# Performance work log

Measured on AMD Instinct MI355X. Metric: run time of the kernel, lower is better.

The kernel has to match this reference:

```python
import jax, jax.numpy as jnp
import numpy as np

BIG = 1000000.0
EPS = 1e-06
COST_CLASS, COST_BBOX, COST_GIOU = 1.0, 5.0, 2.0


def sanitize_boxes(boxes):
    # boxes: [..., 4] cxcywh
    boxes = jnp.nan_to_num(boxes, nan=0.0, posinf=1.0, neginf=0.0)
    cx, cy, w, h = jnp.moveaxis(boxes, -1, 0)
    cx = jnp.clip(cx, 0.0, 1.0)
    cy = jnp.clip(cy, 0.0, 1.0)
    w = jnp.clip(w, EPS, 1.0)
    h = jnp.clip(h, EPS, 1.0)
    return jnp.stack([cx, cy, w, h], axis=-1)


def box_cxcywh_to_xyxy(x):
    cx, cy, w, h = jnp.moveaxis(x, -1, 0)
    return jnp.stack([cx - 0.5 * w, cy - 0.5 * h, cx + 0.5 * w, cy + 0.5 * h], axis=-1)


def pairwise_giou(b1, b2):
    # b1: [B, Q, 4] xyxy, b2: [B, T, 4] xyxy -> [B, Q, T]
    area1 = (b1[..., 2] - b1[..., 0]) * (b1[..., 3] - b1[..., 1])  # [B,Q]
    area2 = (b2[..., 2] - b2[..., 0]) * (b2[..., 3] - b2[..., 1])  # [B,T]
    lt = jnp.maximum(b1[:, :, None, :2], b2[:, None, :, :2])  # [B,Q,T,2]
    rb = jnp.minimum(b1[:, :, None, 2:], b2[:, None, :, 2:])
    wh = jnp.clip(rb - lt, 0.0)
    inter = wh[..., 0] * wh[..., 1]  # [B,Q,T]
    union = area1[:, :, None] + area2[:, None, :] - inter
    iou = inter / union
    # enclosing box
    lt_c = jnp.minimum(b1[:, :, None, :2], b2[:, None, :, :2])
    rb_c = jnp.maximum(b1[:, :, None, 2:], b2[:, None, :, 2:])
    wh_c = jnp.clip(rb_c - lt_c, 0.0)
    area_c = wh_c[..., 0] * wh_c[..., 1]
    return iou - (area_c - union) / area_c


def reference(pred_logits, pred_boxes, tgt_labels, tgt_boxes):
    # Batched cost-matrix construction of HungarianMatcher.forward.
    out_logits = jnp.nan_to_num(pred_logits, nan=0.0, posinf=0.0, neginf=0.0)
    out_prob = jax.nn.softmax(out_logits, axis=-1)  # [B,Q,C]
    out_bbox = sanitize_boxes(pred_boxes)           # [B,Q,4]
    t_bbox = sanitize_boxes(tgt_boxes)              # [B,T,4]

    # cost_class[b,q,t] = -out_prob[b,q,tgt_labels[b,t]]
    B, Q, C = out_prob.shape
    T = tgt_labels.shape[1]
    gather_idx = jnp.broadcast_to(tgt_labels[:, None, :], (B, Q, T))
    cost_class = -jnp.take_along_axis(out_prob, gather_idx, axis=2)  # [B,Q,T]

    # L1 cdist in cxcywh space
    cost_bbox = jnp.sum(jnp.abs(out_bbox[:, :, None, :] - t_bbox[:, None, :, :]), axis=-1)

    cost_giou = -pairwise_giou(box_cxcywh_to_xyxy(out_bbox), box_cxcywh_to_xyxy(t_bbox))

    Cmat = COST_CLASS * cost_class + COST_BBOX * cost_bbox + COST_GIOU * cost_giou
    return jnp.nan_to_num(Cmat, nan=BIG, posinf=BIG, neginf=BIG)


def setup_inputs() -> dict:
    key = jax.random.key(0)
    k1, k2, k3, k4 = jax.random.split(key, 4)
    B, Q, C, T = 64, 900, 256, 200
    return {
        "pred_logits": jax.random.normal(k1, (B, Q, C), dtype=jnp.float32),
        "pred_boxes": jax.random.uniform(k2, (B, Q, 4), dtype=jnp.float32),
        "tgt_labels": jax.random.randint(k3, (B, T), 0, C),
        "tgt_boxes": jax.random.uniform(k4, (B, T, 4), dtype=jnp.float32),
    }
```

## Files before the change

### kernel.cpp

```cpp
#include <hip/hip_runtime.h>
#include <math.h>

constexpr int B = 64, Q = 900, C = 256, T = 200;
constexpr float BIG = 1000000.0f;
constexpr float EPSV = 1e-6f;
constexpr int WAVES_PER_BLOCK = 4;
constexpr int QPB = WAVES_PER_BLOCK;

__device__ __forceinline__ float fix_logit(float x) {
    unsigned u = __float_as_uint(x);
    return ((u & 0x7f800000u) == 0x7f800000u) ? 0.0f : x;
}

__device__ __forceinline__ float fix_box(float x) {
    unsigned u = __float_as_uint(x);
    if ((u & 0x7f800000u) == 0x7f800000u) {
        if (u & 0x007fffffu) return 0.0f;
        return (u & 0x80000000u) ? 0.0f : 1.0f;
    }
    return x;
}

__device__ __forceinline__ float clampf(float x, float lo, float hi) {
    return fminf(fmaxf(x, lo), hi);
}

__global__ __launch_bounds__(256, 2)
void matcher_kernel(const float* __restrict__ logits,
                    const float* __restrict__ pboxes,
                    const int*   __restrict__ tlabels,
                    const float* __restrict__ tboxes,
                    float* __restrict__ out)
{
    __shared__ float s_tx0[T], s_ty0[T], s_tx1[T], s_ty1[T], s_tarea[T];
    __shared__ float s_tcx[T], s_tcy[T], s_tw[T], s_th[T];
    __shared__ int   s_tlab[T];
    __shared__ float s_exp[WAVES_PER_BLOCK][C];

    const int blocks_per_b = Q / QPB;
    const int b    = blockIdx.x / blocks_per_b;
    const int qblk = blockIdx.x % blocks_per_b;
    const int tid  = threadIdx.x;
    const int wave = tid >> 6;
    const int lane = tid & 63;
    const int q    = qblk * QPB + wave;

    for (int t = tid; t < T; t += blockDim.x) {
        float4 tb = ((const float4*)(tboxes + (size_t)b * T * 4))[t];
        float cx = clampf(fix_box(tb.x), 0.0f, 1.0f);
        float cy = clampf(fix_box(tb.y), 0.0f, 1.0f);
        float w  = clampf(fix_box(tb.z), EPSV, 1.0f);
        float h  = clampf(fix_box(tb.w), EPSV, 1.0f);
        s_tcx[t] = cx; s_tcy[t] = cy; s_tw[t] = w; s_th[t] = h;
        float x0 = cx - 0.5f * w, y0 = cy - 0.5f * h;
        float x1 = cx + 0.5f * w, y1 = cy + 0.5f * h;
        s_tx0[t] = x0; s_ty0[t] = y0; s_tx1[t] = x1; s_ty1[t] = y1;
        s_tarea[t] = (x1 - x0) * (y1 - y0);
        int lab = tlabels[(size_t)b * T + t];
        s_tlab[t] = min(max(lab, 0), C - 1);
    }

    const size_t row = (size_t)b * Q + q;
    const float4 lg4 = ((const float4*)(logits + row * C))[lane];
    float l0 = fix_logit(lg4.x), l1 = fix_logit(lg4.y);
    float l2 = fix_logit(lg4.z), l3 = fix_logit(lg4.w);

    float m = fmaxf(fmaxf(l0, l1), fmaxf(l2, l3));
    #pragma unroll
    for (int off = 32; off > 0; off >>= 1)
        m = fmaxf(m, __shfl_xor(m, off));

    float e0 = __expf(l0 - m), e1 = __expf(l1 - m);
    float e2 = __expf(l2 - m), e3 = __expf(l3 - m);
    float s = (e0 + e1) + (e2 + e3);
    #pragma unroll
    for (int off = 32; off > 0; off >>= 1)
        s += __shfl_xor(s, off);
    const float inv_sum = 1.0f / s;

    ((float4*)&s_exp[wave][0])[lane] = make_float4(e0, e1, e2, e3);

    const float4 pb = *(const float4*)(pboxes + row * 4);
    float pcx = clampf(fix_box(pb.x), 0.0f, 1.0f);
    float pcy = clampf(fix_box(pb.y), 0.0f, 1.0f);
    float pw  = clampf(fix_box(pb.z), EPSV, 1.0f);
    float ph  = clampf(fix_box(pb.w), EPSV, 1.0f);
    float px0 = pcx - 0.5f * pw, py0 = pcy - 0.5f * ph;
    float px1 = pcx + 0.5f * pw, py1 = pcy + 0.5f * ph;
    float parea = (px1 - px0) * (py1 - py0);

    __syncthreads();

    float* orow = out + row * T;
    for (int t = lane; t < T; t += 64) {
        float prob = s_exp[wave][s_tlab[t]] * inv_sum;

        float l1c = fabsf(pcx - s_tcx[t]) + fabsf(pcy - s_tcy[t])
                  + fabsf(pw  - s_tw[t])  + fabsf(ph  - s_th[t]);

        float ltx = fmaxf(px0, s_tx0[t]), lty = fmaxf(py0, s_ty0[t]);
        float rbx = fminf(px1, s_tx1[t]), rby = fminf(py1, s_ty1[t]);
        float iw = fmaxf(rbx - ltx, 0.0f), ih = fmaxf(rby - lty, 0.0f);
        float inter = iw * ih;
        float uni = parea + s_tarea[t] - inter;
        float iou = inter / uni;

        float cx0 = fminf(px0, s_tx0[t]), cy0 = fminf(py0, s_ty0[t]);
        float cx1 = fmaxf(px1, s_tx1[t]), cy1 = fmaxf(py1, s_ty1[t]);
        float cw = fmaxf(cx1 - cx0, 0.0f), ch = fmaxf(cy1 - cy0, 0.0f);
        float ca = cw * ch;
        float giou = iou - (ca - uni) / ca;

        float cost = -prob + 5.0f * l1c - 2.0f * giou;
        unsigned cu = __float_as_uint(cost);
        if ((cu & 0x7f800000u) == 0x7f800000u) cost = BIG;
        orow[t] = cost;
    }
}

extern "C" void kernel_launch(void* const* d_in, const int* in_sizes, int n_in,
                              void* d_out, int out_size, void* d_ws, size_t ws_size,
                              hipStream_t stream) {
    const float* logits  = (const float*)d_in[0];
    const float* pboxes  = (const float*)d_in[1];
    const int*   tlabels = (const int*)d_in[2];
    const float* tboxes  = (const float*)d_in[3];
    float* out = (float*)d_out;

    dim3 grid(B * (Q / QPB));
    dim3 block(64 * WAVES_PER_BLOCK);
    matcher_kernel<<<grid, block, 0, stream>>>(logits, pboxes, tlabels, tboxes, out);
}
```

Baseline: 123.4 us.

## Process eight queries per wave with target boxes held in registers

Each wave now handles eight query rows instead of one. Target boxes and label offsets are loaded once into per-lane registers, which removes the shared-memory target tables and the block-wide barrier, and amortises target preprocessing across queries. The GIoU and L1 terms are rewritten algebraically into a single reciprocal with fused multiply-adds, using the fast `rcpf` intrinsic. The final NaN/Inf-to-BIG check is dropped, on the assumption that sanitised boxes keep the denominators positive. The costs are slightly different rounding from the approximate reciprocals, and per-wave reuse of the shared softmax buffer with no explicit barrier between iterations.

```diff
diff --git a/kernel.cpp b/kernel.cpp
--- a/kernel.cpp
+++ b/kernel.cpp
@@ -2,10 +2,10 @@
 #include <math.h>
 
 constexpr int B = 64, Q = 900, C = 256, T = 200;
-constexpr float BIG = 1000000.0f;
 constexpr float EPSV = 1e-6f;
-constexpr int WAVES_PER_BLOCK = 4;
-constexpr int QPB = WAVES_PER_BLOCK;
+constexpr int WPB = 4;
+constexpr int QPW = 8;
+constexpr int QPB = WPB * QPW;
 
 __device__ __forceinline__ float fix_logit(float x) {
     unsigned u = __float_as_uint(x);
@@ -25,96 +25,100 @@
     return fminf(fmaxf(x, lo), hi);
 }
 
-__global__ __launch_bounds__(256, 2)
+__global__ __launch_bounds__(256, 4)
 void matcher_kernel(const float* __restrict__ logits,
                     const float* __restrict__ pboxes,
                     const int*   __restrict__ tlabels,
                     const float* __restrict__ tboxes,
                     float* __restrict__ out)
 {
-    __shared__ float s_tx0[T], s_ty0[T], s_tx1[T], s_ty1[T], s_tarea[T];
-    __shared__ float s_tcx[T], s_tcy[T], s_tw[T], s_th[T];
-    __shared__ int   s_tlab[T];
-    __shared__ float s_exp[WAVES_PER_BLOCK][C];
+    __shared__ float s_exp[WPB * C];
 
-    const int blocks_per_b = Q / QPB;
+    const int blocks_per_b = (Q + QPB - 1) / QPB;
     const int b    = blockIdx.x / blocks_per_b;
     const int qblk = blockIdx.x % blocks_per_b;
-    const int tid  = threadIdx.x;
-    const int wave = tid >> 6;
-    const int lane = tid & 63;
-    const int q    = qblk * QPB + wave;
+    const int wave = threadIdx.x >> 6;
+    const int lane = threadIdx.x & 63;
+    const int q0   = qblk * QPB + wave * QPW;
 
-    for (int t = tid; t < T; t += blockDim.x) {
-        float4 tb = ((const float4*)(tboxes + (size_t)b * T * 4))[t];
+    float tx0[4], ty0[4], tx1[4], ty1[4], tw[4], th[4];
+    int   lofs[4];
+    #pragma unroll
+    for (int s = 0; s < 4; ++s) {
+        int t  = lane + 64 * s;
+        int tc = t < T ? t : T - 1;
+        float4 tb = ((const float4*)(tboxes + (size_t)b * T * 4))[tc];
         float cx = clampf(fix_box(tb.x), 0.0f, 1.0f);
         float cy = clampf(fix_box(tb.y), 0.0f, 1.0f);
         float w  = clampf(fix_box(tb.z), EPSV, 1.0f);
         float h  = clampf(fix_box(tb.w), EPSV, 1.0f);
-        s_tcx[t] = cx; s_tcy[t] = cy; s_tw[t] = w; s_th[t] = h;
-        float x0 = cx - 0.5f * w, y0 = cy - 0.5f * h;
-        float x1 = cx + 0.5f * w, y1 = cy + 0.5f * h;
-        s_tx0[t] = x0; s_ty0[t] = y0; s_tx1[t] = x1; s_ty1[t] = y1;
-        s_tarea[t] = (x1 - x0) * (y1 - y0);
-        int lab = tlabels[(size_t)b * T + t];
-        s_tlab[t] = min(max(lab, 0), C - 1);
+        tw[s] = w;  th[s] = h;
+        tx0[s] = cx - 0.5f * w;  ty0[s] = cy - 0.5f * h;
+        tx1[s] = cx + 0.5f * w;  ty1[s] = cy + 0.5f * h;
+        int lab = tlabels[(size_t)b * T + tc];
+        lofs[s] = wave * C + min(max(lab, 0), C - 1);
     }
 
-    const size_t row = (size_t)b * Q + q;
-    const float4 lg4 = ((const float4*)(logits + row * C))[lane];
-    float l0 = fix_logit(lg4.x), l1 = fix_logit(lg4.y);
-    float l2 = fix_logit(lg4.z), l3 = fix_logit(lg4.w);
+    for (int i = 0; i < QPW; ++i) {
+        const int q = q0 + i;
+        if (q >= Q) break;
+        const size_t row = (size_t)b * Q + q;
 
-    float m = fmaxf(fmaxf(l0, l1), fmaxf(l2, l3));
-    #pragma unroll
-    for (int off = 32; off > 0; off >>= 1)
-        m = fmaxf(m, __shfl_xor(m, off));
+        float4 lg = ((const float4*)(logits + row * C))[lane];
+        float l0 = fix_logit(lg.x), l1 = fix_logit(lg.y);
+        float l2 = fix_logit(lg.z), l3 = fix_logit(lg.w);
+        float m = fmaxf(fmaxf(l0, l1), fmaxf(l2, l3));
+        #pragma unroll
+        for (int off = 32; off; off >>= 1) m = fmaxf(m, __shfl_xor(m, off));
+        float e0 = __expf(l0 - m), e1 = __expf(l1 - m);
+        float e2 = __expf(l2 - m), e3 = __expf(l3 - m);
+        float ssum = (e0 + e1) + (e2 + e3);
+        #pragma unroll
+        for (int off = 32; off; off >>= 1) ssum += __shfl_xor(ssum, off);
+        const float inv = __builtin_amdgcn_rcpf(ssum);
+        ((float4*)(s_exp + wave * C))[lane] = make_float4(e0, e1, e2, e3);
 
-    float e0 = __expf(l0 - m), e1 = __expf(l1 - m);
-    float e2 = __expf(l2 - m), e3 = __expf(l3 - m);
-    float s = (e0 + e1) + (e2 + e3);
-    #pragma unroll
-    for (int off = 32; off > 0; off >>= 1)
-        s += __shfl_xor(s, off);
-    const float inv_sum = 1.0f / s;
+        float4 pb = *(const float4*)(pboxes + row * 4);
+        float pcx = clampf(fix_box(pb.x), 0.0f, 1.0f);
+        float pcy = clampf(fix_box(pb.y), 0.0f, 1.0f);
+        float pw  = clampf(fix_box(pb.z), EPSV, 1.0f);
+        float ph  = clampf(fix_box(pb.w), EPSV, 1.0f);
+        float px0 = pcx - 0.5f * pw, py0 = pcy - 0.5f * ph;
+        float px1 = pcx + 0.5f * pw, py1 = pcy + 0.5f * ph;
+        float psx = px0 + px1, psy = py0 + py1;
+        float parea = pw * ph;
 
-    ((float4*)&s_exp[wave][0])[lane] = make_float4(e0, e1, e2, e3);
+        float* orow = out + row * T;
+        #pragma unroll
+        for (int s = 0; s < 4; ++s) {
+            float g  = s_exp[lofs[s]];
+            float t0 = fmaf(-g, inv, 2.0f);
 
-    const float4 pb = *(const float4*)(pboxes + row * 4);
-    float pcx = clampf(fix_box(pb.x), 0.0f, 1.0f);
-    float pcy = clampf(fix_box(pb.y), 0.0f, 1.0f);
-    float pw  = clampf(fix_box(pb.z), EPSV, 1.0f);
-    float ph  = clampf(fix_box(pb.w), EPSV, 1.0f);
-    float px0 = pcx - 0.5f * pw, py0 = pcy - 0.5f * ph;
-    float px1 = pcx + 0.5f * pw, py1 = pcy + 0.5f * ph;
-    float parea = (px1 - px0) * (py1 - py0);
+            float tsx = tx0[s] + tx1[s];
+            float tsy = ty0[s] + ty1[s];
+            float s1 = fabsf(psx - tsx) + fabsf(psy - tsy);
+            float s2 = fabsf(pw - tw[s]) + fabsf(ph - th[s]);
 
-    __syncthreads();
+            float iw = fminf(px1, tx1[s]) - fmaxf(px0, tx0[s]);
+            float ih = fminf(py1, ty1[s]) - fmaxf(py0, ty0[s]);
+            iw = fmaxf(iw, 0.0f);  ih = fmaxf(ih, 0.0f);
+            float inter = iw * ih;
+            float uni = fmaf(tw[s], th[s], parea) - inter;
 
-    float* orow = out + row * T;
-    for (int t = lane; t < T; t += 64) {
-        float prob = s_exp[wave][s_tlab[t]] * inv_sum;
+            float cw = fmaxf(px1, tx1[s]) - fminf(px0, tx0[s]);
+            float ch = fmaxf(py1, ty1[s]) - fminf(py0, ty0[s]);
+            float ca = cw * ch;
 
-        float l1c = fabsf(pcx - s_tcx[t]) + fabsf(pcy - s_tcy[t])
-                  + fabsf(pw  - s_tw[t])  + fabsf(ph  - s_th[t]);
+            float num = fmaf(uni, uni, inter * ca);
+            float val = num * __builtin_amdgcn_rcpf(uni * ca);
 
-        float ltx = fmaxf(px0, s_tx0[t]), lty = fmaxf(py0, s_ty0[t]);
-        float rbx = fminf(px1, s_tx1[t]), rby = fminf(py1, s_ty1[t]);
-        float iw = fmaxf(rbx - ltx, 0.0f), ih = fmaxf(rby - lty, 0.0f);
-        float inter = iw * ih;
-        float uni = parea + s_tarea[t] - inter;
-        float iou = inter / uni;
+            float cost = fmaf(2.5f, s1, t0);
+            cost = fmaf(5.0f, s2, cost);
+            cost = fmaf(-2.0f, val, cost);
 
-        float cx0 = fminf(px0, s_tx0[t]), cy0 = fminf(py0, s_ty0[t]);
-        float cx1 = fmaxf(px1, s_tx1[t]), cy1 = fmaxf(py1, s_ty1[t]);
-        float cw = fmaxf(cx1 - cx0, 0.0f), ch = fmaxf(cy1 - cy0, 0.0f);
-        float ca = cw * ch;
-        float giou = iou - (ca - uni) / ca;
-
-        float cost = -prob + 5.0f * l1c - 2.0f * giou;
-        unsigned cu = __float_as_uint(cost);
-        if ((cu & 0x7f800000u) == 0x7f800000u) cost = BIG;
-        orow[t] = cost;
+            int t = lane + 64 * s;
+            if (t < T) orow[t] = cost;
+        }
     }
 }
 
@@ -127,7 +131,8 @@
     const float* tboxes  = (const float*)d_in[3];
     float* out = (float*)d_out;
 
-    dim3 grid(B * (Q / QPB));
-    dim3 block(64 * WAVES_PER_BLOCK);
+    const int blocks_per_b = (Q + QPB - 1) / QPB;
+    dim3 grid(B * blocks_per_b);
+    dim3 block(64 * WPB);
     matcher_kernel<<<grid, block, 0, stream>>>(logits, pboxes, tlabels, tboxes, out);
 }
```

Result: no change. 121.1 us (-1.8%).
